# Performance work log

Measured on AMD Instinct MI355X. Metric: run time of the kernel, lower is better.

## Reference

```python
import jax, jax.numpy as jnp
import numpy as np

# dims derived from init_kwargs
N_NODES = 100000            # type_mask.shape[0]
N0, N1 = 60000, 40000       # nodes per type
F0, F1 = 128, 64            # feats_dim_list
HID = 64                    # hidden_dim (= in_dim of layer1)
HEADS = 8
OUT = 16
ATTN_VEC = 128
E = 250000                  # metapath instances per metapath
L = 3                       # nodes per metapath instance (2 edge types)
NG = 8192                   # nodes in each minibatch DGL graph
B = 8192                    # number of target nodes
ETYPES = [[0, 1], [2, 3]]   # etypes_list; num_edge_type=4, RotatE0 -> 2 base relations


def setup_inputs() -> dict:
    ks = jax.random.split(jax.random.key(0), 20)
    g = lambda k, s, sc=1.0: sc * jax.random.normal(k, s, dtype=jnp.float32)
    return {
        "feat0": g(ks[0], (N0, F0)),
        "feat1": g(ks[1], (N1, F1)),
        "W0": g(ks[2], (HID, F0), 0.12),
        "b0": jnp.zeros((HID,), jnp.float32),
        "W1": g(ks[3], (HID, F1), 0.15),
        "b1": jnp.zeros((HID,), jnp.float32),
        "r_vec": g(ks[4], (2, HID // 2, 2), 0.2),
        "attn0": g(ks[5], (HEADS, HID), 0.2),
        "attn1": g(ks[6], (HEADS, HID), 0.2),
        "fc1_w": g(ks[7], (ATTN_VEC, HEADS * HID), 0.06),
        "fc1_b": jnp.zeros((ATTN_VEC,), jnp.float32),
        "fc2_w": g(ks[8], (1, ATTN_VEC), 0.1),
        "fc_w": g(ks[9], (OUT, HEADS * HID), 0.06),
        "fc_b": jnp.zeros((OUT,), jnp.float32),
        "idx0": jnp.arange(N0, dtype=jnp.int32),                 # type-0 node ids (contiguous block)
        "idx1": jnp.arange(N1, dtype=jnp.int32) + N0,            # type-1 node ids (offset block)
        "mp0_indices": jax.random.randint(ks[10], (E, L), 0, N_NODES, dtype=jnp.int32),
        "mp0_dst": jax.random.randint(ks[11], (E,), 0, NG, dtype=jnp.int32),
        "mp0_target": jax.random.randint(ks[12], (B,), 0, NG, dtype=jnp.int32),
        "mp1_indices": jax.random.randint(ks[13], (E, L), 0, N_NODES, dtype=jnp.int32),
        "mp1_dst": jax.random.randint(ks[14], (E,), 0, NG, dtype=jnp.int32),
        "mp1_target": jax.random.randint(ks[15], (B,), 0, NG, dtype=jnp.int32),
    }


def _cmul(a, b):
    # complex multiply on trailing dim of size 2
    re = a[..., 0] * b[..., 0] - a[..., 1] * b[..., 1]
    im = a[..., 0] * b[..., 1] + a[..., 1] * b[..., 0]
    return jnp.stack([re, im], axis=-1)


def reference(feat0, feat1, W0, b0, W1, b1, r_vec, attn0, attn1,
              fc1_w, fc1_b, fc2_w, fc_w, fc_b,
              idx0, idx1,
              mp0_indices, mp0_dst, mp0_target,
              mp1_indices, mp1_dst, mp1_target):
    # per-node-type linear scattered into a dense [N, HID] table (dropout=0 / eval)
    tf = jnp.zeros((N_NODES, HID), jnp.float32)
    tf = tf.at[idx0].set(feat0 @ W0.T + b0)
    tf = tf.at[idx1].set(feat1 @ W1.T + b1)

    # RotatE0: unit-modulus normalize, then double relations with conjugates
    rv = r_vec / jnp.linalg.norm(r_vec, axis=-1, keepdims=True)          # [2, HID//2, 2]
    conj = rv * jnp.array([1.0, -1.0], rv.dtype)
    rv_full = jnp.stack([rv, conj], axis=1).reshape(-1, HID // 2, 2)     # [4, HID//2, 2]

    def metapath(indices, dst, target, attn, etypes):
        edata = tf[indices].reshape(E, L, HID // 2, 2)   # gather metapath instances
        # suffix products of rotations: final[i] = prod_{j>=i} r[etypes[j]], final[L-1]=1
        final = [jnp.stack([jnp.ones(HID // 2, jnp.float32),
                            jnp.zeros(HID // 2, jnp.float32)], -1)]
        for i in range(L - 2, -1, -1):
            final.insert(0, _cmul(final[0], rv_full[etypes[i]]))
        finals = jnp.stack(final, axis=0)                # [L, HID//2, 2]
        edata = _cmul(edata, finals)                     # rotate every path position
        h = edata.reshape(E, L, HID).mean(axis=1)        # [E, HID] instance encoding
        # node-level attention (heads share h: torch tiles hidden across heads)
        a = jax.nn.leaky_relu(h @ attn.T, 0.01)          # [E, HEADS]
        m = jax.ops.segment_max(a, dst, num_segments=NG)
        ex = jnp.exp(a - m[dst])
        s = jax.ops.segment_sum(ex, dst, num_segments=NG)
        an = ex / s[dst]                                 # edge softmax per destination
        eft = jnp.einsum('eh,ed->ehd', an, h)            # [E, HEADS, HID]
        ft = jax.ops.segment_sum(eft, dst, num_segments=NG)
        ret = ft[target].reshape(B, HEADS * HID)
        return jax.nn.elu(ret)

    out0 = metapath(mp0_indices, mp0_dst, mp0_target, attn0, ETYPES[0])
    out1 = metapath(mp1_indices, mp1_dst, mp1_target, attn1, ETYPES[1])

    # metapath-level attention
    outs = jnp.stack([out0, out1], axis=0)               # [P, B, HEADS*HID]
    s1 = jnp.tanh(outs @ fc1_w.T + fc1_b)                # [P, B, ATTN_VEC]
    beta = jax.nn.softmax((s1.mean(axis=1) @ fc2_w.T)[:, 0], axis=0)  # [P]
    hagg = jnp.einsum('p,pbf->bf', beta, outs)           # [B, HEADS*HID]
    logits = hagg @ fc_w.T + fc_b                        # [B, OUT]
    return logits, hagg
```

## Files before the change

kernel.cpp:

```cpp
#include <hip/hip_runtime.h>
#include <hip/hip_fp16.h>
#include <math.h>

#define NNODES 100000
#define NT0 60000
#define NT1 40000
#define FD0 128
#define FD1 64
#define HID 64
#define HEADS 8
#define OUTD 16
#define AVEC 128
#define NE 250000
#define NG 8192
#define NB 8192

typedef _Float16 half8v __attribute__((ext_vector_type(8)));
typedef float f32x4 __attribute__((ext_vector_type(4)));

#define OFF_TF16    0ull
#define OFF_FINALS  3200000ull
#define OFF_ACC     3200512ull
#define OFF_BETA    3200768ull
#define OFF_WC0     3201024ull
#define OFF_WC1     3208192ull
#define OFF_BC0     3211776ull
#define OFF_BC1     3211904ull
#define OFF_FC1H    3212032ull
#define OFF_P       3244800ull
#define OFF_SORTED  5644800ull
#define OFF_COUNTS  7644800ull
#define OFF_CNTT    7661184ull
#define OFF_CURS    7677568ull
#define OFF_OFFS    7693952ull
#define OFF_FT16    7710592ull
#define OFF_L       11904896ull
#define OFF_FCWH    12167040ull

#define NB_TF0 ((NT0 + 63)/64)
#define NB_TF1 ((NT1 + 63)/64)
#define NB_TF  (NB_TF0 + NB_TF1)
#define NB_SC  ((2*NE + 255)/256)

__device__ __forceinline__ float2 rot_pair(const float* r_vec, int pi, int j){
  const float2* rv = (const float2*)r_vec;
  int rel = pi >= 3 ? 1 : 0;
  float2 r = rv[rel*32 + j];
  float n = rsqrtf(r.x*r.x + r.y*r.y);
  r.x *= n; r.y *= n;
  float2 rf = make_float2(r.x, -r.y);
  int pos = pi - rel*3;
  if (pos == 2) return make_float2(1.f, 0.f);
  if (pos == 1) return rf;
  return make_float2(rf.x*r.x - rf.y*r.y, rf.x*r.y + rf.y*r.x);
}

__global__ __launch_bounds__(128) void k_wcat(const float* __restrict__ r_vec,
     const float* __restrict__ attn0, const float* __restrict__ attn1,
     const float* __restrict__ W0v, const float* __restrict__ b0v,
     const float* __restrict__ W1v, const float* __restrict__ b1v,
     const float* __restrict__ fc1_w, const float* __restrict__ fc_w,
     __half* __restrict__ wc0, float* __restrict__ bc0,
     __half* __restrict__ wc1, float* __restrict__ bc1,
     __half* __restrict__ fc1h, __half* __restrict__ fcwh,
     int* __restrict__ counts,
     float* __restrict__ finals, float* __restrict__ acc){
  int bid = blockIdx.x;
  int t = threadIdx.x;
  if (bid == 297){
    for (int i = t; i < OUTD*512; i += 128) fcwh[i] = __float2half(fc_w[i]);
    return;
  }
  if (bid >= 289){
    int base = (bid - 289)*4096;
    #pragma unroll
    for (int i = t; i < 4096; i += 128) counts[base + i] = 0;
    return;
  }
  if (bid == 288){
    if (t < 32){
      float2* F = (float2*)finals;
      #pragma unroll
      for (int pi = 0; pi < 6; ++pi) F[pi*32 + t] = rot_pair(r_vec, pi, t);
    }
    for (int q = t; q < 256; q += 128) acc[q] = 0.f;
    return;
  }
  if (bid >= 224){
    int base = (bid - 224)*1024;
    for (int i = t; i < 1024; i += 128)
      fc1h[base + i] = __float2half(fc1_w[base + i]);
    return;
  }
  int type = bid >= 112;
  int c = bid - type*112;
  int F = type ? FD1 : FD0;
  const float* W  = type ? W1v : W0v;
  const float* bv = type ? b1v : b0v;
  __half* wc = type ? wc1 : wc0;
  float* bc  = type ? bc1 : bc0;

  if (c < 64){
    for (int f = t; f < F; f += 128) wc[(size_t)c*F + f] = __float2half(W[(size_t)c*F + f]);
    if (t == 0) bc[c] = bv[c];
    return;
  }
  __shared__ float a[64];
  int cg = c - 64;
  int pi = cg >> 3, k = cg & 7;
  if (t < 32){
    float2 f = rot_pair(r_vec, pi, t);
    const float* at = (pi >= 3) ? attn1 : attn0;
    float a0 = at[k*64 + 2*t], a1 = at[k*64 + 2*t + 1];
    a[2*t]     = (f.x*a0 + f.y*a1) * (1.f/3.f);
    a[2*t + 1] = (f.x*a1 - f.y*a0) * (1.f/3.f);
  }
  __syncthreads();
  for (int f = t; f < F; f += 128){
    float s = 0.f;
    #pragma unroll 16
    for (int d = 0; d < 64; ++d) s += a[d] * W[(size_t)d*F + f];
    wc[(size_t)c*F + f] = __float2half(s);
  }
  if (t == 0){
    float s = 0.f;
    #pragma unroll 16
    for (int d = 0; d < 64; ++d) s += a[d] * bv[d];
    bc[c] = s;
  }
}

__global__ void k_hist3(const int* __restrict__ d0, const int* __restrict__ d1,
                        const int* __restrict__ t0, const int* __restrict__ t1,
                        int* __restrict__ counts, int* __restrict__ cntt){
  int e = blockIdx.x*blockDim.x + threadIdx.x;
  if (e < NE) atomicAdd(&counts[d0[e]], 1);
  else if (e < 2*NE) atomicAdd(&counts[NG + d1[e-NE]], 1);
  else if (e < 2*NE + NB) atomicAdd(&cntt[t0[e-2*NE]], 1);
  else if (e < 2*NE + 2*NB) atomicAdd(&cntt[NG + t1[e-2*NE-NB]], 1);
}

__global__ __launch_bounds__(1024) void k_scan(const int* __restrict__ counts,
                                               int* __restrict__ offs,
                                               int* __restrict__ curs){
  __shared__ int lds[1024];
  int t = threadIdx.x;
  int base = t*16;
  int v[16]; int sum = 0;
  #pragma unroll
  for (int i = 0; i < 16; ++i){ v[i] = counts[base+i]; sum += v[i]; }
  lds[t] = sum;
  __syncthreads();
  for (int off = 1; off < 1024; off <<= 1){
    int x = (t >= off) ? lds[t-off] : 0;
    __syncthreads();
    lds[t] += x;
    __syncthreads();
  }
  int excl = lds[t] - sum;
  #pragma unroll
  for (int i = 0; i < 16; ++i){ offs[base+i] = excl; excl += v[i]; curs[base+i] = 0; }
  if (t == 1023) offs[2*NG] = excl;
}

__global__ __launch_bounds__(256) void k_mid(const float* __restrict__ feat0,
      const int* __restrict__ idx0, const float* __restrict__ feat1,
      const int* __restrict__ idx1,
      const __half* __restrict__ wc0, const float* __restrict__ bc0,
      const __half* __restrict__ wc1, const float* __restrict__ bc1,
      const int* __restrict__ m0, const int* __restrict__ d0,
      const int* __restrict__ m1, const int* __restrict__ d1,
      const int* __restrict__ offs, int* __restrict__ curs,
      int4* __restrict__ sorted,
      __half* __restrict__ tf16, __half* __restrict__ P){
  int bid = blockIdx.x;
  int t = threadIdx.x;
  if (bid >= NB_TF){
    int e = (bid - NB_TF)*256 + t;
    if (e >= 2*NE) return;
    const int* mp; int d;
    if (e < NE){ mp = m0 + (size_t)e*3; d = d0[e]; }
    else { mp = m1 + (size_t)(e-NE)*3; d = NG + d1[e-NE]; }
    int pos = offs[d] + atomicAdd(&curs[d], 1);
    sorted[pos] = make_int4(mp[0], mp[1], mp[2], 0);
    return;
  }
  const float* feat; const int* idx; const __half* wc; const float* bc;
  int n_nodes, F, m0b;
  if (bid < NB_TF0){ feat=feat0; idx=idx0; wc=wc0; bc=bc0; n_nodes=NT0; F=FD0; m0b=bid*64; }
  else { feat=feat1; idx=idx1; wc=wc1; bc=bc1; n_nodes=NT1; F=FD1; m0b=(bid-NB_TF0)*64; }
  __shared__ int idxs[64];
  __shared__ __half outs[64][120];
  if (t < 64){
    int gm = m0b + t; if (gm > n_nodes - 1) gm = n_nodes - 1;
    idxs[t] = idx[gm];
  }
  __syncthreads();
  int w = t >> 6, l = t & 63;
  int lr = l & 15, lk = l >> 4;
  int gr = m0b + w*16 + lr; if (gr > n_nodes - 1) gr = n_nodes - 1;
  const float* arow = feat + (size_t)gr*F;

  f32x4 acc7[7];
  #pragma unroll
  for (int ct = 0; ct < 7; ++ct) acc7[ct] = (f32x4){0.f,0.f,0.f,0.f};

  int nk = F >> 5;
  for (int kk = 0; kk < nk; ++kk){
    int koff = kk*32 + lk*8;
    float4 ua = *(const float4*)(arow + koff);
    float4 ub = *(const float4*)(arow + koff + 4);
    half8v a = {(_Float16)ua.x,(_Float16)ua.y,(_Float16)ua.z,(_Float16)ua.w,
                (_Float16)ub.x,(_Float16)ub.y,(_Float16)ub.z,(_Float16)ub.w};
    #pragma unroll
    for (int ct = 0; ct < 7; ++ct){
      half8v b = *(const half8v*)(wc + (size_t)(ct*16 + lr)*F + koff);
      acc7[ct] = __builtin_amdgcn_mfma_f32_16x16x32_f16(a, b, acc7[ct], 0, 0, 0);
    }
  }

  #pragma unroll
  for (int ct = 0; ct < 7; ++ct){
    int col = ct*16 + lr;
    float bvv = bc[col];
    #pragma unroll
    for (int r = 0; r < 4; ++r){
      int nl = w*16 + lk*4 + r;
      outs[nl][col] = __float2half(acc7[ct][r] + bvv);
    }
  }
  __syncthreads();
  #pragma unroll
  for (int u = t; u < 512; u += 256){
    int n = u >> 3, c = u & 7;
    if (m0b + n < n_nodes){
      uint4 v = *(uint4*)&outs[n][c*8];
      *(uint4*)&tf16[(size_t)idxs[n]*64 + c*8] = v;
    }
  }
  for (int u = t; u < 384; u += 256){
    int pp = u >= 192;
    int rr = u - pp*192;
    int n = rr / 3, c = rr - n*3;
    if (m0b + n < n_nodes){
      uint4 v = *(uint4*)&outs[n][64 + pp*24 + c*8];
      *(uint4*)&P[(size_t)pp*2400000 + (size_t)idxs[n]*24 + c*8] = v;
    }
  }
}

__global__ __launch_bounds__(128) void k_seg(const __half* __restrict__ tf16,
                                             const __half* __restrict__ P,
                                             const int4* __restrict__ sorted,
                                             const int* __restrict__ offs,
                                             const float* __restrict__ finals,
                                             __half* __restrict__ ft16o){
  __shared__ int4 ndb[2][64];
  __shared__ float wb[2][64][8];
  int wv = threadIdx.x >> 6;
  int seg = blockIdx.x*2 + wv;
  int p = seg >> 13;
  int lane = threadIdx.x & 63;
  int hw = lane >> 5, j = lane & 31;
  int start = offs[seg], end = offs[seg+1];
  __half2* ftw = (__half2*)(ft16o + (size_t)seg*512);
  if (start == end){
    #pragma unroll
    for (int kk = 0; kk < 4; ++kk) ftw[(hw*4+kk)*32 + j] = __floats2half2_rn(0.f, 0.f);
    return;
  }
  const float2* F2 = (const float2*)(finals + p*192);
  float2 f0 = F2[j], f1 = F2[32 + j];
  const __half2* tfh = (const __half2*)tf16;
  const __half* Pp = P + (size_t)p*2400000;
  int4* nb = ndb[wv];
  float (*wbp)[8] = wb[wv];

  float sA[8], ur[8], ui[8];
  #pragma unroll
  for (int k = 0; k < 8; ++k){ sA[k] = 0.f; ur[k] = 0.f; ui[k] = 0.f; }

  for (int c = start; c < end; c += 64){
    int n = end - c; if (n > 64) n = 64;
    if (lane < n){
      int4 nd = sorted[c + lane];
      nb[lane] = nd;
      float4 rA = *(const float4*)(Pp + (size_t)nd.x*24);
      float4 rB = *(const float4*)(Pp + (size_t)nd.y*24 + 8);
      float4 rC = *(const float4*)(Pp + (size_t)nd.z*24 + 16);
      const __half2* ha = (const __half2*)&rA;
      const __half2* hb = (const __half2*)&rB;
      const __half2* hc = (const __half2*)&rC;
      float w[8];
      #pragma unroll
      for (int m = 0; m < 4; ++m){
        float2 va = __half22float2(ha[m]);
        float2 vb = __half22float2(hb[m]);
        float2 vc = __half22float2(hc[m]);
        float x0 = va.x + vb.x + vc.x;
        float x1 = va.y + vb.y + vc.y;
        x0 = x0 > 0.f ? x0 : 0.01f*x0;
        x1 = x1 > 0.f ? x1 : 0.01f*x1;
        w[2*m]   = __expf(x0);
        w[2*m+1] = __expf(x1);
      }
      #pragma unroll
      for (int k = 0; k < 8; ++k) sA[k] += w[k];
      *(float4*)&wbp[lane][0] = make_float4(w[0], w[1], w[2], w[3]);
      *(float4*)&wbp[lane][4] = make_float4(w[4], w[5], w[6], w[7]);
    }
    asm volatile("s_waitcnt lgkmcnt(0)" ::: "memory");
    __builtin_amdgcn_sched_barrier(0);
    int cend = c + n;
    #pragma unroll 2
    for (int i = c + hw; i < cend; i += 2){
      int e = i - c;
      int4 nd = nb[e];
      float4 wlo = *(const float4*)&wbp[e][0];
      float4 whi = *(const float4*)&wbp[e][4];
      float2 v0 = __half22float2(tfh[(size_t)nd.x*32 + j]);
      float2 v1 = __half22float2(tfh[(size_t)nd.y*32 + j]);
      float2 v2 = __half22float2(tfh[(size_t)nd.z*32 + j]);
      float hre = (v0.x*f0.x - v0.y*f0.y) + (v1.x*f1.x - v1.y*f1.y) + v2.x;
      float him = (v0.x*f0.y + v0.y*f0.x) + (v1.x*f1.y + v1.y*f1.x) + v2.y;
      ur[0] += wlo.x*hre; ui[0] += wlo.x*him;
      ur[1] += wlo.y*hre; ui[1] += wlo.y*him;
      ur[2] += wlo.z*hre; ui[2] += wlo.z*him;
      ur[3] += wlo.w*hre; ui[3] += wlo.w*him;
      ur[4] += whi.x*hre; ui[4] += whi.x*him;
      ur[5] += whi.y*hre; ui[5] += whi.y*him;
      ur[6] += whi.z*hre; ui[6] += whi.z*him;
      ur[7] += whi.w*hre; ui[7] += whi.w*him;
    }
    asm volatile("s_waitcnt lgkmcnt(0)" ::: "memory");
    __builtin_amdgcn_sched_barrier(0);
  }
  #pragma unroll
  for (int k = 0; k < 8; ++k){
    ur[k] += __shfl_xor(ur[k], 32);
    ui[k] += __shfl_xor(ui[k], 32);
    float v = sA[k];
    #pragma unroll
    for (int mask = 1; mask < 64; mask <<= 1) v += __shfl_xor(v, mask);
    sA[k] = v;
  }
  #pragma unroll
  for (int kk = 0; kk < 4; ++kk){
    int k = hw*4 + kk;
    float inv = 1.f / (3.f * sA[k]);
    float re = ur[k]*inv, im = ui[k]*inv;
    re = re > 0.f ? re : expm1f(re);
    im = im > 0.f ? im : expm1f(im);
    ftw[k*32 + j] = __floats2half2_rn(re, im);
  }
}

__global__ __launch_bounds__(256) void k_s1g(const __half* __restrict__ ft16o,
                                             const int* __restrict__ cntt,
                                             const __half* __restrict__ fc1h,
                                             const float* __restrict__ fc1_b,
                                             const __half* __restrict__ fcwh,
                                             float* __restrict__ Lb,
                                             float* __restrict__ acc_p){
  int bid = blockIdx.x;
  int p  = bid >> 8;
  int rb = bid & 255;
  int t = threadIdx.x;
  int w = t >> 6, l = t & 63;
  int rowbase = rb*32 + (w & 1)*16;
  int colbase = (w >> 1)*64;
  int lr = l & 15, lk = l >> 4;
  bool doL = (w >> 1) == 0;

  const half8v* Ab = (const half8v*)(ft16o + ((size_t)p*NG + rowbase)*512);
  f32x4 acc[4] = {{0.f,0.f,0.f,0.f},{0.f,0.f,0.f,0.f},
                  {0.f,0.f,0.f,0.f},{0.f,0.f,0.f,0.f}};
  f32x4 accL = {0.f,0.f,0.f,0.f};

  #pragma unroll 4
  for (int kk = 0; kk < 16; ++kk){
    half8v a = Ab[(size_t)lr*64 + kk*4 + lk];
    #pragma unroll
    for (int ct = 0; ct < 4; ++ct){
      const half8v* Bb = (const half8v*)(fc1h + (size_t)(colbase + ct*16 + lr)*512);
      half8v b = Bb[kk*4 + lk];
      acc[ct] = __builtin_amdgcn_mfma_f32_16x16x32_f16(a, b, acc[ct], 0, 0, 0);
    }
    if (doL){
      half8v b = *(const half8v*)(fcwh + (size_t)lr*512 + kk*32 + lk*8);
      accL = __builtin_amdgcn_mfma_f32_16x16x32_f16(a, b, accL, 0, 0, 0);
    }
  }

  float cf[4];
  #pragma unroll
  for (int r = 0; r < 4; ++r)
    cf[r] = (float)cntt[p*NG + rowbase + lk*4 + r];
  #pragma unroll
  for (int ct = 0; ct < 4; ++ct){
    int col = colbase + ct*16 + lr;
    float bv = fc1_b[col];
    float sv = 0.f;
    #pragma unroll
    for (int r = 0; r < 4; ++r)
      sv += cf[r] * tanhf(acc[ct][r] + bv);
    sv += __shfl_xor(sv, 16);
    sv += __shfl_xor(sv, 32);
    if (l < 16) atomicAdd(&acc_p[p*128 + col], sv);
  }
  if (doL){
    #pragma unroll
    for (int r = 0; r < 4; ++r)
      Lb[((size_t)p*NG + rowbase + lk*4 + r)*16 + lr] = accL[r];
  }
}

__global__ void k_final(const __half* __restrict__ ft0, const __half* __restrict__ ft1,
                        const int* __restrict__ tgt0, const int* __restrict__ tgt1,
                        const float* __restrict__ acc, const float* __restrict__ fc2_w,
                        const float* __restrict__ Lb, const float* __restrict__ fc_b,
                        float* __restrict__ d_out){
  __shared__ float bsh[2];
  int b = blockIdx.x, t = threadIdx.x;
  if (t < 64){
    float s0 = acc[t]*fc2_w[t] + acc[t+64]*fc2_w[t+64];
    float s1 = acc[128+t]*fc2_w[t] + acc[192+t]*fc2_w[t+64];
    #pragma unroll
    for (int mask = 1; mask < 64; mask <<= 1){
      s0 += __shfl_xor(s0, mask, 64);
      s1 += __shfl_xor(s1, mask, 64);
    }
    if (t == 0){
      float z0 = s0 / (float)NB, z1 = s1 / (float)NB;
      float mz = fmaxf(z0, z1);
      float e0 = expf(z0 - mz), e1 = expf(z1 - mz);
      float inv = 1.f / (e0 + e1);
      bsh[0] = e0*inv; bsh[1] = e1*inv;
    }
  }
  __syncthreads();
  float b0 = bsh[0], b1 = bsh[1];
  int g0 = tgt0[b], g1 = tgt1[b];
  float v0 = __half2float(ft0[(size_t)g0*512 + t]);
  float v1 = __half2float(ft1[(size_t)g1*512 + t]);
  d_out[(size_t)NB*OUTD + (size_t)b*512 + t] = b0*v0 + b1*v1;
  if (t < OUTD){
    float lv = b0*Lb[(size_t)g0*16 + t] + b1*Lb[((size_t)NG + g1)*16 + t] + fc_b[t];
    d_out[(size_t)b*OUTD + t] = lv;
  }
}

extern "C" void kernel_launch(void* const* d_in, const int* in_sizes, int n_in,
                              void* d_out, int out_size, void* d_ws, size_t ws_size,
                              hipStream_t stream){
  const float* feat0  = (const float*)d_in[0];
  const float* feat1  = (const float*)d_in[1];
  const float* W0     = (const float*)d_in[2];
  const float* b0     = (const float*)d_in[3];
  const float* W1     = (const float*)d_in[4];
  const float* b1     = (const float*)d_in[5];
  const float* r_vec  = (const float*)d_in[6];
  const float* attn0  = (const float*)d_in[7];
  const float* attn1  = (const float*)d_in[8];
  const float* fc1_w  = (const float*)d_in[9];
  const float* fc1_b  = (const float*)d_in[10];
  const float* fc2_w  = (const float*)d_in[11];
  const float* fc_w   = (const float*)d_in[12];
  const float* fc_b   = (const float*)d_in[13];
  const int*   idx0   = (const int*)d_in[14];
  const int*   idx1   = (const int*)d_in[15];
  const int*   mpi0   = (const int*)d_in[16];
  const int*   mdst0  = (const int*)d_in[17];
  const int*   mtgt0  = (const int*)d_in[18];
  const int*   mpi1   = (const int*)d_in[19];
  const int*   mdst1  = (const int*)d_in[20];
  const int*   mtgt1  = (const int*)d_in[21];

  float* ws      = (float*)d_ws;
  __half* tf16   = (__half*)(ws + OFF_TF16);
  float* finals  = ws + OFF_FINALS;
  float* acc     = ws + OFF_ACC;
  __half* wc0    = (__half*)(ws + OFF_WC0);
  __half* wc1    = (__half*)(ws + OFF_WC1);
  float* bc0     = ws + OFF_BC0;
  float* bc1     = ws + OFF_BC1;
  __half* fc1h   = (__half*)(ws + OFF_FC1H);
  __half* P      = (__half*)(ws + OFF_P);
  int4*  sorted  = (int4*)(ws + OFF_SORTED);
  int*   counts  = (int*)(ws + OFF_COUNTS);
  int*   cntt    = (int*)(ws + OFF_CNTT);
  int*   curs    = (int*)(ws + OFF_CURS);
  int*   offs    = (int*)(ws + OFF_OFFS);
  __half* ft16o  = (__half*)(ws + OFF_FT16);
  __half* ft0h   = ft16o;
  __half* ft1h   = ft16o + (size_t)NG*512;
  float* Lb      = ws + OFF_L;
  __half* fcwh   = (__half*)(ws + OFF_FCWH);

  k_wcat<<<298, 128, 0, stream>>>(r_vec, attn0, attn1, W0, b0, W1, b1,
                                  fc1_w, fc_w, wc0, bc0, wc1, bc1, fc1h, fcwh,
                                  counts, finals, acc);
  k_hist3<<<(2*NE + 2*NB + 255)/256, 256, 0, stream>>>(mdst0, mdst1, mtgt0, mtgt1,
                                                       counts, cntt);
  k_scan<<<1, 1024, 0, stream>>>(counts, offs, curs);
  k_mid<<<NB_TF + NB_SC, 256, 0, stream>>>(feat0, idx0, feat1, idx1,
                                           wc0, bc0, wc1, bc1,
                                           mpi0, mdst0, mpi1, mdst1,
                                           offs, curs, sorted, tf16, P);
  k_seg<<<NG, 128, 0, stream>>>(tf16, P, sorted, offs, finals, ft16o);
  k_s1g<<<512, 256, 0, stream>>>(ft16o, cntt, fc1h, fc1_b, fcwh, Lb, acc);
  k_final<<<NB, 512, 0, stream>>>(ft0h, ft1h, mtgt0, mtgt1, acc, fc2_w, Lb, fc_b,
                                  (float*)d_out);
}
```

Baseline: 210.9 us.

## Merge histogram into weight-prep kernel and pad P rows to 32 halves

The separate histogram kernel is folded into k_wcat as extra blocks. Zeroing of counts moves to a hipMemsetAsync before the launch, which removes one kernel launch and lets the atomics overlap the weight precompute. The P projection table is also padded from 24 to 32 halves per node so each row is 64-byte aligned, which should make the gathered loads in k_seg cheaper. The cost is a larger P buffer and an extra memset call, and all workspace offsets are shifted to fit.

```diff
diff --git a/kernel.cpp b/kernel.cpp
--- a/kernel.cpp
+++ b/kernel.cpp
@@ -28,19 +28,22 @@
 #define OFF_BC1     3211904ull
 #define OFF_FC1H    3212032ull
 #define OFF_P       3244800ull
-#define OFF_SORTED  5644800ull
-#define OFF_COUNTS  7644800ull
-#define OFF_CNTT    7661184ull
-#define OFF_CURS    7677568ull
-#define OFF_OFFS    7693952ull
-#define OFF_FT16    7710592ull
-#define OFF_L       11904896ull
-#define OFF_FCWH    12167040ull
+#define OFF_SORTED  6444800ull
+#define OFF_COUNTS  8444800ull
+#define OFF_CNTT    8461184ull
+#define OFF_CURS    8477568ull
+#define OFF_OFFS    8493952ull
+#define OFF_FT16    8510592ull
+#define OFF_L       12704896ull
+#define OFF_FCWH    12967040ull
 
 #define NB_TF0 ((NT0 + 63)/64)
 #define NB_TF1 ((NT1 + 63)/64)
 #define NB_TF  (NB_TF0 + NB_TF1)
 #define NB_SC  ((2*NE + 255)/256)
+#define NB_HIST ((2*NE + 2*NB + 127)/128)
+#define PSTRIDE 32
+#define PBASE   3200000
 
 __device__ __forceinline__ float2 rot_pair(const float* r_vec, int pi, int j){
   const float2* rv = (const float2*)r_vec;
@@ -60,21 +63,25 @@
      const float* __restrict__ W0v, const float* __restrict__ b0v,
      const float* __restrict__ W1v, const float* __restrict__ b1v,
      const float* __restrict__ fc1_w, const float* __restrict__ fc_w,
+     const int* __restrict__ d0, const int* __restrict__ d1,
+     const int* __restrict__ t0, const int* __restrict__ t1,
      __half* __restrict__ wc0, float* __restrict__ bc0,
      __half* __restrict__ wc1, float* __restrict__ bc1,
      __half* __restrict__ fc1h, __half* __restrict__ fcwh,
-     int* __restrict__ counts,
+     int* __restrict__ counts, int* __restrict__ cntt,
      float* __restrict__ finals, float* __restrict__ acc){
   int bid = blockIdx.x;
   int t = threadIdx.x;
-  if (bid == 297){
+  if (bid >= 290){
+    int e = (bid - 290)*128 + t;
+    if (e < NE) atomicAdd(&counts[d0[e]], 1);
+    else if (e < 2*NE) atomicAdd(&counts[NG + d1[e-NE]], 1);
+    else if (e < 2*NE + NB) atomicAdd(&cntt[t0[e-2*NE]], 1);
+    else if (e < 2*NE + 2*NB) atomicAdd(&cntt[NG + t1[e-2*NE-NB]], 1);
+    return;
+  }
+  if (bid == 289){
     for (int i = t; i < OUTD*512; i += 128) fcwh[i] = __float2half(fc_w[i]);
-    return;
-  }
-  if (bid >= 289){
-    int base = (bid - 289)*4096;
-    #pragma unroll
-    for (int i = t; i < 4096; i += 128) counts[base + i] = 0;
     return;
   }
   if (bid == 288){
@@ -128,16 +135,6 @@
     for (int d = 0; d < 64; ++d) s += a[d] * bv[d];
     bc[c] = s;
   }
-}
-
-__global__ void k_hist3(const int* __restrict__ d0, const int* __restrict__ d1,
-                        const int* __restrict__ t0, const int* __restrict__ t1,
-                        int* __restrict__ counts, int* __restrict__ cntt){
-  int e = blockIdx.x*blockDim.x + threadIdx.x;
-  if (e < NE) atomicAdd(&counts[d0[e]], 1);
-  else if (e < 2*NE) atomicAdd(&counts[NG + d1[e-NE]], 1);
-  else if (e < 2*NE + NB) atomicAdd(&cntt[t0[e-2*NE]], 1);
-  else if (e < 2*NE + 2*NB) atomicAdd(&cntt[NG + t1[e-2*NE-NB]], 1);
 }
 
 __global__ __launch_bounds__(1024) void k_scan(const int* __restrict__ counts,
@@ -238,13 +235,15 @@
       *(uint4*)&tf16[(size_t)idxs[n]*64 + c*8] = v;
     }
   }
-  for (int u = t; u < 384; u += 256){
-    int pp = u >= 192;
-    int rr = u - pp*192;
-    int n = rr / 3, c = rr - n*3;
+  #pragma unroll
+  for (int u = t; u < 512; u += 256){
+    int pp = u >= 256;
+    int rr = u & 255;
+    int n = rr >> 2, c = rr & 3;
     if (m0b + n < n_nodes){
-      uint4 v = *(uint4*)&outs[n][64 + pp*24 + c*8];
-      *(uint4*)&P[(size_t)pp*2400000 + (size_t)idxs[n]*24 + c*8] = v;
+      int srcc = c < 3 ? c : 2;
+      uint4 v = *(uint4*)&outs[n][64 + pp*24 + srcc*8];
+      *(uint4*)&P[(size_t)pp*PBASE + (size_t)idxs[n]*PSTRIDE + c*8] = v;
     }
   }
 }
@@ -272,7 +271,7 @@
   const float2* F2 = (const float2*)(finals + p*192);
   float2 f0 = F2[j], f1 = F2[32 + j];
   const __half2* tfh = (const __half2*)tf16;
-  const __half* Pp = P + (size_t)p*2400000;
+  const __half* Pp = P + (size_t)p*PBASE;
   int4* nb = ndb[wv];
   float (*wbp)[8] = wb[wv];
 
@@ -285,9 +284,9 @@
     if (lane < n){
       int4 nd = sorted[c + lane];
       nb[lane] = nd;
-      float4 rA = *(const float4*)(Pp + (size_t)nd.x*24);
-      float4 rB = *(const float4*)(Pp + (size_t)nd.y*24 + 8);
-      float4 rC = *(const float4*)(Pp + (size_t)nd.z*24 + 16);
+      float4 rA = *(const float4*)(Pp + (size_t)nd.x*PSTRIDE);
+      float4 rB = *(const float4*)(Pp + (size_t)nd.y*PSTRIDE + 8);
+      float4 rC = *(const float4*)(Pp + (size_t)nd.z*PSTRIDE + 16);
       const __half2* ha = (const __half2*)&rA;
       const __half2* hb = (const __half2*)&rB;
       const __half2* hc = (const __half2*)&rC;
@@ -497,11 +496,11 @@
   float* Lb      = ws + OFF_L;
   __half* fcwh   = (__half*)(ws + OFF_FCWH);
 
-  k_wcat<<<298, 128, 0, stream>>>(r_vec, attn0, attn1, W0, b0, W1, b1,
-                                  fc1_w, fc_w, wc0, bc0, wc1, bc1, fc1h, fcwh,
-                                  counts, finals, acc);
-  k_hist3<<<(2*NE + 2*NB + 255)/256, 256, 0, stream>>>(mdst0, mdst1, mtgt0, mtgt1,
-                                                       counts, cntt);
+  hipMemsetAsync(counts, 0, 2*16384*sizeof(int), stream);
+  k_wcat<<<290 + NB_HIST, 128, 0, stream>>>(r_vec, attn0, attn1, W0, b0, W1, b1,
+                                            fc1_w, fc_w, mdst0, mdst1, mtgt0, mtgt1,
+                                            wc0, bc0, wc1, bc1, fc1h, fcwh,
+                                            counts, cntt, finals, acc);
   k_scan<<<1, 1024, 0, stream>>>(counts, offs, curs);
   k_mid<<<NB_TF + NB_SC, 256, 0, stream>>>(feat0, idx0, feat1, idx1,
                                            wc0, bc0, wc1, bc1,
```

New measurement: 212.3 us. About the same (+0.7%).
